# Optimization experiments

Measured on AMD Instinct MI355X. Metric: run time of the kernel, lower is better.

The kernel has to match this reference:

```python
import math
import jax, jax.numpy as jnp
import numpy as np

B, N, D = 8, 1024, 1024


def setup_inputs() -> dict:
    key = jax.random.key(0)
    ks = jax.random.split(key, 5)
    scale = 1.0 / math.sqrt(D)  # ~torch Linear init scale
    x = jax.random.normal(ks[0], (B, N, D), jnp.float32)
    Wq = jax.random.uniform(ks[1], (D, D), jnp.float32, -scale, scale)
    Wk = jax.random.uniform(ks[2], (D, D), jnp.float32, -scale, scale)
    Wv = jax.random.uniform(ks[3], (D, D), jnp.float32, -scale, scale)
    Ws = jax.random.uniform(ks[4], (D, 1), jnp.float32, -scale, scale)
    return {"x": x, "Wq": Wq, "Wk": Wk, "Wv": Wv, "Ws": Ws}


def reference(x, Wq, Wk, Wv, Ws):
    # projections
    Q = x @ Wq                      # [B, N, D]
    K = x @ Wk
    V = x @ Wv
    sigma = x @ Ws                  # [B, N, 1]
    sigma = jax.nn.sigmoid(sigma * 5.0) + 1e-5
    sigma = jnp.power(3.0, sigma) - 1.0

    # prior association: Gaussian kernel over |i-j| distances
    idx = jnp.arange(N, dtype=jnp.float32)
    dist = jnp.abs(idx[:, None] - idx[None, :])            # [N, N]
    inv_norm = 1.0 / (jnp.sqrt(2.0 * jnp.pi) * sigma)      # [B, N, 1]
    gaussian = inv_norm * jnp.exp(-0.5 * jnp.square(dist / sigma))  # [B, N, N]
    P = gaussian / gaussian.sum(axis=(1, 2), keepdims=True)

    # series association: softmax over the BATCH dim (dim=0), as in source
    scores = jnp.einsum('bnd,bmd->bnm', Q, K) / math.sqrt(D)  # [B, N, N]
    S = jax.nn.softmax(scores, axis=0)

    # reconstruction
    Z = jnp.einsum('bnm,bmd->bnd', S, V)                     # [B, N, D]
    return Z, P
```

## Files before the change

kernel.cpp:

```cpp
#include <hip/hip_runtime.h>


typedef __attribute__((ext_vector_type(8))) short bf16x8;
typedef __attribute__((ext_vector_type(4))) float f32x4;
typedef unsigned short ushort_t;

#define DI __device__ __forceinline__

constexpr long NN = 1024L * 1024L;
constexpr long ND = 1024L * 1024L;

DI ushort_t f2bf(float f) {
    unsigned int u = __float_as_uint(f);
    u = u + 0x7fffu + ((u >> 16) & 1u);
    return (ushort_t)(u >> 16);
}

template <int OUT_BF16>
DI void g3b_body(const ushort_t* __restrict__ Ab, const ushort_t* __restrict__ Bb,
                 void* __restrict__ Cb, int ldA, int ldB, int ldC,
                 float scale, int bx, int by, ushort_t* lds)
{
    constexpr int BUF   = 24576;
    constexpr int B_OFF = 8192;

    const int tid  = threadIdx.x;
    const int wave = tid >> 6;
    const int lane = tid & 63;
    const int wm   = wave >> 2;
    const int wn   = wave & 3;
    const int gm   = bx * 128;
    const int gn   = by * 256;

    const int srow = tid >> 3;
    const int scol = 8 * ((tid & 7) ^ (srow & 7));
    const int sdst = wave * 512;

    auto stageA = [&](int t, int d, int h) {
        const ushort_t* src = Ab + (long)(gm + h * 64 + srow) * ldA + t * 64 + scol;
        __builtin_amdgcn_global_load_lds(
            (const __attribute__((address_space(1))) void*)src,
            (__attribute__((address_space(3))) void*)(&lds[d * BUF + h * 4096 + sdst]),
            16, 0, 0);
    };
    auto stageB = [&](int t, int d, int h, int j) {
        const ushort_t* src = Bb + (long)(gn + h * 128 + j * 64 + srow) * ldB + t * 64 + scol;
        __builtin_amdgcn_global_load_lds(
            (const __attribute__((address_space(1))) void*)src,
            (__attribute__((address_space(3))) void*)(&lds[d * BUF + B_OFF + h * 8192 + j * 4096 + sdst]),
            16, 0, 0);
    };

    const int arow = wm * 64 + (lane & 15);
    const int brow = wn * 64 + (lane & 15);
    const int cs0 = (((lane >> 4) * 16) ^ ((lane & 7) << 4)) >> 1;
    const int cs1 = ((64 + (lane >> 4) * 16) ^ ((lane & 7) << 4)) >> 1;

    f32x4 acc[4][4];
#pragma unroll
    for (int m = 0; m < 4; ++m)
#pragma unroll
        for (int n = 0; n < 4; ++n) acc[m][n] = (f32x4){0.f, 0.f, 0.f, 0.f};

    stageA(0, 0, 0); stageA(0, 0, 1);
    stageB(0, 0, 0, 0); stageB(0, 0, 0, 1); stageB(0, 0, 1, 0); stageB(0, 0, 1, 1);
    stageA(1, 1, 0); stageA(1, 1, 1);
    stageB(1, 1, 0, 0); stageB(1, 1, 0, 1); stageB(1, 1, 1, 0); stageB(1, 1, 1, 1);
    asm volatile("s_waitcnt vmcnt(6)" ::: "memory");
    __builtin_amdgcn_s_barrier();
    __builtin_amdgcn_sched_barrier(0);

    int cur = 0;
    for (int t = 0; t < 16; ++t) {
        const int nxt = (cur == 0) ? 2 : cur - 1;
        const ushort_t* la = &lds[cur * BUF];
        const ushort_t* lb = &lds[cur * BUF + B_OFF];

        bf16x8 a[2][4], b[2][4];
#pragma unroll
        for (int mi = 0; mi < 4; ++mi) {
            a[0][mi] = *(const bf16x8*)&la[(arow + mi * 16) * 64 + cs0];
            a[1][mi] = *(const bf16x8*)&la[(arow + mi * 16) * 64 + cs1];
        }
#pragma unroll
        for (int ni = 0; ni < 2; ++ni) {
            b[0][ni] = *(const bf16x8*)&lb[(brow + ni * 16) * 64 + cs0];
            b[1][ni] = *(const bf16x8*)&lb[(brow + ni * 16) * 64 + cs1];
        }
        if (t < 14) {
            stageB(t + 2, nxt, 0, 0); stageB(t + 2, nxt, 0, 1);
            stageB(t + 2, nxt, 1, 0); stageB(t + 2, nxt, 1, 1);
        }
        __builtin_amdgcn_s_barrier();
        asm volatile("s_waitcnt lgkmcnt(0)" ::: "memory");
        __builtin_amdgcn_sched_barrier(0);
        __builtin_amdgcn_s_setprio(1);
#pragma unroll
        for (int mi = 0; mi < 4; ++mi)
#pragma unroll
            for (int ni = 0; ni < 2; ++ni) {
                acc[mi][ni] = __builtin_amdgcn_mfma_f32_16x16x32_bf16(a[0][mi], b[0][ni], acc[mi][ni], 0, 0, 0);
                acc[mi][ni] = __builtin_amdgcn_mfma_f32_16x16x32_bf16(a[1][mi], b[1][ni], acc[mi][ni], 0, 0, 0);
            }
        __builtin_amdgcn_s_setprio(0);
        __builtin_amdgcn_s_barrier();
        __builtin_amdgcn_sched_barrier(0);

#pragma unroll
        for (int ni = 2; ni < 4; ++ni) {
            b[0][ni] = *(const bf16x8*)&lb[(brow + ni * 16) * 64 + cs0];
            b[1][ni] = *(const bf16x8*)&lb[(brow + ni * 16) * 64 + cs1];
        }
        if (t < 14) { stageA(t + 2, nxt, 0); stageA(t + 2, nxt, 1); }
        __builtin_amdgcn_s_barrier();
        asm volatile("s_waitcnt lgkmcnt(0)" ::: "memory");
        if (t < 14) asm volatile("s_waitcnt vmcnt(6)" ::: "memory");
        else        asm volatile("s_waitcnt vmcnt(0)" ::: "memory");
        __builtin_amdgcn_sched_barrier(0);
        __builtin_amdgcn_s_setprio(1);
#pragma unroll
        for (int mi = 0; mi < 4; ++mi)
#pragma unroll
            for (int ni = 2; ni < 4; ++ni) {
                acc[mi][ni] = __builtin_amdgcn_mfma_f32_16x16x32_bf16(a[0][mi], b[0][ni], acc[mi][ni], 0, 0, 0);
                acc[mi][ni] = __builtin_amdgcn_mfma_f32_16x16x32_bf16(a[1][mi], b[1][ni], acc[mi][ni], 0, 0, 0);
            }
        __builtin_amdgcn_s_setprio(0);
        __builtin_amdgcn_s_barrier();
        __builtin_amdgcn_sched_barrier(0);

        cur = (cur == 2) ? 0 : cur + 1;
    }

    if (OUT_BF16) {
        ushort_t* el = lds;
#pragma unroll
        for (int mi = 0; mi < 4; ++mi)
#pragma unroll
            for (int ni = 0; ni < 4; ++ni)
#pragma unroll
                for (int r = 0; r < 4; ++r)
                    el[(wm * 64 + mi * 16 + (lane >> 4) * 4 + r) * 256 +
                       wn * 64 + ni * 16 + (lane & 15)] = f2bf(acc[mi][ni][r] * scale);
        __builtin_amdgcn_s_barrier();
        ushort_t* C = (ushort_t*)Cb;
#pragma unroll
        for (int rr = 0; rr < 8; ++rr) {
            const int row = rr * 16 + (tid >> 5);
            const int col = (tid & 31) * 8;
            *(bf16x8*)&C[(long)(gm + row) * ldC + gn + col] =
                *(const bf16x8*)&el[row * 256 + col];
        }
    } else {
        float* el = (float*)lds;
        float* C  = (float*)Cb;
#pragma unroll
        for (int h = 0; h < 2; ++h) {
            if (wm == h) {
#pragma unroll
                for (int mi = 0; mi < 4; ++mi)
#pragma unroll
                    for (int ni = 0; ni < 4; ++ni)
#pragma unroll
                        for (int r = 0; r < 4; ++r)
                            el[(mi * 16 + (lane >> 4) * 4 + r) * 256 +
                               wn * 64 + ni * 16 + (lane & 15)] = acc[mi][ni][r] * scale;
            }
            __builtin_amdgcn_s_barrier();
#pragma unroll
            for (int i = 0; i < 8; ++i) {
                const int cc  = i * 512 + tid;
                const int row = cc >> 6;
                const int c4  = (cc & 63) * 4;
                *(float4*)&C[(long)(gm + h * 64 + row) * ldC + gn + c4] =
                    *(const float4*)&el[row * 256 + c4];
            }
            __builtin_amdgcn_s_barrier();
        }
    }
}

template <int OUT_BF16>
__global__ __launch_bounds__(512, 2)
void gemm3b(const ushort_t* __restrict__ A, const ushort_t* __restrict__ B,
            void* __restrict__ Cout, int ldA, int ldB, int ldC,
            long sA, long sB, long sC, float scale,
            int n0, int n1, int xfirst)
{
    __shared__ ushort_t lds[3 * 24576];
    const int total = gridDim.x;
    const int lin   = blockIdx.x;
    const int swz   = (lin & 7) * (total >> 3) + (lin >> 3);
    const int c0    = swz % n0;
    const int rem   = swz / n0;
    const int c1    = rem % n1;
    const int bz    = rem / n1;
    const int bx    = xfirst ? c0 : c1;
    const int by    = xfirst ? c1 : c0;
    void* Cb = OUT_BF16 ? (void*)((ushort_t*)Cout + (long)bz * sC)
                        : (void*)((float*)Cout + (long)bz * sC);
    g3b_body<OUT_BF16>(A + (long)bz * sA, B + (long)bz * sB, Cb,
                       ldA, ldB, ldC, scale, bx, by, lds);
}

template <int OUT_BF16>
DI void g256_body(const ushort_t* __restrict__ Ab, const ushort_t* __restrict__ Bb,
                  void* __restrict__ Cb, int ldA, int ldB, int ldC,
                  float scale, int bx, int by, ushort_t* ldsp)
{
    constexpr int BUF   = 32768;
    constexpr int B_OFF = 16384;

    const int tid  = threadIdx.x;
    const int wave = tid >> 6;
    const int lane = tid & 63;
    const int wm   = wave >> 2;
    const int wn   = wave & 3;
    const int gm   = bx * 256;
    const int gn   = by * 256;

    const int srow = tid >> 3;
    const int scol = 8 * ((tid & 7) ^ (srow & 7));
    const int sdst = wave * 512;

    auto stage = [&](int t, int d, int op, int h) {
        const ushort_t* g  = op ? Bb : Ab;
        const int       ld = op ? ldB : ldA;
        const int       g0 = (op ? gn : gm) + h * 128;
#pragma unroll
        for (int j = 0; j < 2; ++j) {
            const ushort_t* src = g + (long)(g0 + j * 64 + srow) * ld + t * 64 + scol;
            __builtin_amdgcn_global_load_lds(
                (const __attribute__((address_space(1))) void*)src,
                (__attribute__((address_space(3))) void*)
                    (&ldsp[d * BUF + op * B_OFF + h * 8192 + j * 4096 + sdst]),
                16, 0, 0);
        }
    };

    const int arow = wm * 128 + (lane & 15);
    const int brow = wn * 64 + (lane & 15);
    const int cs0 = (((lane >> 4) * 16) ^ ((lane & 7) << 4)) >> 1;
    const int cs1 = ((64 + (lane >> 4) * 16) ^ ((lane & 7) << 4)) >> 1;

    f32x4 acc[8][4];
#pragma unroll
    for (int m = 0; m < 8; ++m)
#pragma unroll
        for (int n = 0; n < 4; ++n) acc[m][n] = (f32x4){0.f, 0.f, 0.f, 0.f};

    stage(0, 0, 0, 0); stage(0, 0, 0, 1); stage(0, 0, 1, 0); stage(0, 0, 1, 1);
    stage(1, 1, 0, 0); stage(1, 1, 0, 1); stage(1, 1, 1, 0); stage(1, 1, 1, 1);
    asm volatile("s_waitcnt vmcnt(8)" ::: "memory");
    __builtin_amdgcn_s_barrier();
    __builtin_amdgcn_sched_barrier(0);

    bf16x8 a[2][4], b0[2][2], b1[2][2];
#pragma unroll 2
    for (int t = 0; t < 16; ++t) {
        const int cur = t & 1;
        const ushort_t* la = &ldsp[cur * BUF];
        const ushort_t* lb = &ldsp[cur * BUF + B_OFF];

#pragma unroll
        for (int mi = 0; mi < 4; ++mi) {
            a[0][mi] = *(const bf16x8*)&la[(arow + mi * 16) * 64 + cs0];
            a[1][mi] = *(const bf16x8*)&la[(arow + mi * 16) * 64 + cs1];
        }
#pragma unroll
        for (int ni = 0; ni < 2; ++ni) {
            b0[0][ni] = *(const bf16x8*)&lb[(brow + ni * 16) * 64 + cs0];
            b0[1][ni] = *(const bf16x8*)&lb[(brow + ni * 16) * 64 + cs1];
        }
        __builtin_amdgcn_s_barrier();
        asm volatile("s_waitcnt lgkmcnt(0)" ::: "memory");
        __builtin_amdgcn_sched_barrier(0);
        __builtin_amdgcn_s_setprio(1);
#pragma unroll
        for (int mi = 0; mi < 4; ++mi)
#pragma unroll
            for (int ni = 0; ni < 2; ++ni) {
                acc[mi][ni] = __builtin_amdgcn_mfma_f32_16x16x32_bf16(a[0][mi], b0[0][ni], acc[mi][ni], 0, 0, 0);
                acc[mi][ni] = __builtin_amdgcn_mfma_f32_16x16x32_bf16(a[1][mi], b0[1][ni], acc[mi][ni], 0, 0, 0);
            }
        __builtin_amdgcn_s_setprio(0);
        __builtin_amdgcn_s_barrier();
        __builtin_amdgcn_sched_barrier(0);

#pragma unroll
        for (int ni = 0; ni < 2; ++ni) {
            b1[0][ni] = *(const bf16x8*)&lb[(brow + (ni + 2) * 16) * 64 + cs0];
            b1[1][ni] = *(const bf16x8*)&lb[(brow + (ni + 2) * 16) * 64 + cs1];
        }
        __builtin_amdgcn_s_barrier();
        asm volatile("s_waitcnt lgkmcnt(0)" ::: "memory");
        __builtin_amdgcn_sched_barrier(0);
        __builtin_amdgcn_s_setprio(1);
#pragma unroll
        for (int mi = 0; mi < 4; ++mi)
#pragma unroll
            for (int ni = 0; ni < 2; ++ni) {
                acc[mi][ni + 2] = __builtin_amdgcn_mfma_f32_16x16x32_bf16(a[0][mi], b1[0][ni], acc[mi][ni + 2], 0, 0, 0);
                acc[mi][ni + 2] = __builtin_amdgcn_mfma_f32_16x16x32_bf16(a[1][mi], b1[1][ni], acc[mi][ni + 2], 0, 0, 0);
            }
        __builtin_amdgcn_s_setprio(0);
        __builtin_amdgcn_s_barrier();
        __builtin_amdgcn_sched_barrier(0);

#pragma unroll
        for (int mi = 0; mi < 4; ++mi) {
            a[0][mi] = *(const bf16x8*)&la[(arow + (mi + 4) * 16) * 64 + cs0];
            a[1][mi] = *(const bf16x8*)&la[(arow + (mi + 4) * 16) * 64 + cs1];
        }
        if (t < 14) { stage(t + 2, cur, 1, 0); stage(t + 2, cur, 1, 1); }
        __builtin_amdgcn_s_barrier();
        asm volatile("s_waitcnt lgkmcnt(0)" ::: "memory");
        __builtin_amdgcn_sched_barrier(0);
        __builtin_amdgcn_s_setprio(1);
#pragma unroll
        for (int mi = 0; mi < 4; ++mi)
#pragma unroll
            for (int ni = 0; ni < 2; ++ni) {
                acc[mi + 4][ni + 2] = __builtin_amdgcn_mfma_f32_16x16x32_bf16(a[0][mi], b1[0][ni], acc[mi + 4][ni + 2], 0, 0, 0);
                acc[mi + 4][ni + 2] = __builtin_amdgcn_mfma_f32_16x16x32_bf16(a[1][mi], b1[1][ni], acc[mi + 4][ni + 2], 0, 0, 0);
            }
        __builtin_amdgcn_s_setprio(0);
        __builtin_amdgcn_s_barrier();
        __builtin_amdgcn_sched_barrier(0);

        if (t < 14) { stage(t + 2, cur, 0, 0); stage(t + 2, cur, 0, 1); }
        if (t < 14)       asm volatile("s_waitcnt vmcnt(8)" ::: "memory");
        else if (t == 14) asm volatile("s_waitcnt vmcnt(0)" ::: "memory");
        __builtin_amdgcn_sched_barrier(0);
        __builtin_amdgcn_s_setprio(1);
#pragma unroll
        for (int mi = 0; mi < 4; ++mi)
#pragma unroll
            for (int ni = 0; ni < 2; ++ni) {
                acc[mi + 4][ni] = __builtin_amdgcn_mfma_f32_16x16x32_bf16(a[0][mi], b0[0][ni], acc[mi + 4][ni], 0, 0, 0);
                acc[mi + 4][ni] = __builtin_amdgcn_mfma_f32_16x16x32_bf16(a[1][mi], b0[1][ni], acc[mi + 4][ni], 0, 0, 0);
            }
        __builtin_amdgcn_s_setprio(0);
        __builtin_amdgcn_s_barrier();
        __builtin_amdgcn_sched_barrier(0);
    }

    if (OUT_BF16) {
        ushort_t* el = ldsp;
#pragma unroll
        for (int mi = 0; mi < 8; ++mi)
#pragma unroll
            for (int ni = 0; ni < 4; ++ni)
#pragma unroll
                for (int r = 0; r < 4; ++r)
                    el[(wm * 128 + mi * 16 + (lane >> 4) * 4 + r) * 256 +
                       wn * 64 + ni * 16 + (lane & 15)] = f2bf(acc[mi][ni][r] * scale);
        __builtin_amdgcn_s_barrier();
        ushort_t* C = (ushort_t*)Cb;
#pragma unroll
        for (int i = 0; i < 16; ++i) {
            const int cc  = i * 512 + tid;
            const int row = cc >> 5;
            const int col = (cc & 31) * 8;
            *(bf16x8*)&C[(long)(gm + row) * ldC + gn + col] =
                *(const bf16x8*)&el[row * 256 + col];
        }
    } else {
        float* el = (float*)ldsp;
        float* C  = (float*)Cb;
#pragma unroll
        for (int h = 0; h < 2; ++h) {
            if (wm == h) {
#pragma unroll
                for (int mi = 0; mi < 8; ++mi)
#pragma unroll
                    for (int ni = 0; ni < 4; ++ni)
#pragma unroll
                        for (int r = 0; r < 4; ++r)
                            el[(mi * 16 + (lane >> 4) * 4 + r) * 256 +
                               wn * 64 + ni * 16 + (lane & 15)] = acc[mi][ni][r] * scale;
            }
            __builtin_amdgcn_s_barrier();
#pragma unroll
            for (int i = 0; i < 16; ++i) {
                const int cc  = i * 512 + tid;
                const int row = cc >> 6;
                const int c4  = (cc & 63) * 4;
                *(float4*)&C[(long)(gm + h * 128 + row) * ldC + gn + c4] =
                    *(const float4*)&el[row * 256 + c4];
            }
            __builtin_amdgcn_s_barrier();
        }
    }
}

__global__ __launch_bounds__(512)
void prep_g(const float* __restrict__ x, const float* __restrict__ Ws,
            const float* __restrict__ Wq, const float* __restrict__ Wk,
            const float* __restrict__ Wv,
            ushort_t* __restrict__ xh, float* __restrict__ sigma,
            float* __restrict__ rowsum,
            ushort_t* __restrict__ WvT, ushort_t* __restrict__ G)
{
    __shared__ char smem[20608];
    const int blk = blockIdx.x;
    const int tid = threadIdx.x;

    if (blk < 160) {
        const int wave = tid >> 6, lane = tid & 63;
        for (int row = blk * 8 + wave; row < 8192; row += 1280) {
            const float* xr = x + (long)row * 1024;
            float dot = 0.f;
#pragma unroll
            for (int c = 0; c < 4; ++c) {
                const int i = c * 256 + lane * 4;
                float4 v = *(const float4*)(xr + i);
                float4 w = *(const float4*)(Ws + i);
                dot += v.x * w.x + v.y * w.y + v.z * w.z + v.w * w.w;
                ushort4 o;
                o.x = f2bf(v.x); o.y = f2bf(v.y); o.z = f2bf(v.z); o.w = f2bf(v.w);
                *(ushort4*)(xh + (long)row * 1024 + i) = o;
            }
#pragma unroll
            for (int o = 32; o; o >>= 1) dot += __shfl_down(dot, o);
            float sg;
            if (lane == 0) {
                float s = 1.f / (1.f + __expf(-5.f * dot)) + 1e-5f;
                sg = exp2f(s * 1.5849625007211562f) - 1.f;
            }
            sg = __shfl(sg, 0);
            const int i = row & 1023;
            const float c = -0.5f / (sg * sg);
            float a = 0.f;
            for (int j = lane; j < 1024; j += 64) {
                float d = (float)(i - j);
                a += __expf(c * d * d);
            }
#pragma unroll
            for (int o = 32; o; o >>= 1) a += __shfl_down(a, o);
            if (lane == 0) {
                sigma[row]  = sg;
                rowsum[row] = (0.3989422804014327f / sg) * a;
            }
        }
    } else if (blk < 192) {
        float (*s)[65] = (float(*)[65])smem;
        const int r = tid >> 4, c4 = (tid & 15) * 4;
#pragma unroll
        for (int it = 0; it < 8; ++it) {
            const int tile = (blk - 160) * 8 + it;
            const int tr = (tile >> 4) * 64, tc = (tile & 15) * 64;
#pragma unroll
            for (int rr = r; rr < 64; rr += 32) {
                float4 v = *(const float4*)(Wv + (long)(tr + rr) * 1024 + tc + c4);
                s[rr][c4] = v.x; s[rr][c4 + 1] = v.y; s[rr][c4 + 2] = v.z; s[rr][c4 + 3] = v.w;
            }
            __syncthreads();
#pragma unroll
            for (int rr = r; rr < 64; rr += 32) {
                ushort4 o;
                o.x = f2bf(s[c4][rr]);     o.y = f2bf(s[c4 + 1][rr]);
                o.z = f2bf(s[c4 + 2][rr]); o.w = f2bf(s[c4 + 3][rr]);
                *(ushort4*)(WvT + (long)(tc + rr) * 1024 + tr + c4) = o;
            }
            __syncthreads();
        }
    } else {
        ushort_t* sA = (ushort_t*)smem;
        ushort_t* sB = sA + 5120;
        const int g  = blk - 192;
        const int gm = (g >> 3) * 128, gn = (g & 7) * 128;
        const int wave = tid >> 6, lane = tid & 63;
        const int wm = wave >> 2, wn = wave & 3;
        const int lrow = tid >> 3, lcol = (tid & 7) * 4;
        const float* A0 = Wk + (long)(gm + lrow) * 1024 + lcol;
        const float* A1 = Wk + (long)(gm + 64 + lrow) * 1024 + lcol;
        const float* B0 = Wq + (long)(gn + lrow) * 1024 + lcol;
        const float* B1 = Wq + (long)(gn + 64 + lrow) * 1024 + lcol;

        f32x4 acc[4][2];
#pragma unroll
        for (int m = 0; m < 4; ++m)
#pragma unroll
            for (int n = 0; n < 2; ++n) acc[m][n] = (f32x4){0.f, 0.f, 0.f, 0.f};

        auto wr = [&](float4 a0, float4 a1, float4 b0, float4 b1) {
            ushort4 o;
            o.x = f2bf(a0.x); o.y = f2bf(a0.y); o.z = f2bf(a0.z); o.w = f2bf(a0.w);
            *(ushort4*)&sA[lrow * 40 + lcol] = o;
            o.x = f2bf(a1.x); o.y = f2bf(a1.y); o.z = f2bf(a1.z); o.w = f2bf(a1.w);
            *(ushort4*)&sA[(64 + lrow) * 40 + lcol] = o;
            o.x = f2bf(b0.x); o.y = f2bf(b0.y); o.z = f2bf(b0.z); o.w = f2bf(b0.w);
            *(ushort4*)&sB[lrow * 40 + lcol] = o;
            o.x = f2bf(b1.x); o.y = f2bf(b1.y); o.z = f2bf(b1.z); o.w = f2bf(b1.w);
            *(ushort4*)&sB[(64 + lrow) * 40 + lcol] = o;
        };
        auto mm = [&]() {
            bf16x8 af[4], bfv[2];
#pragma unroll
            for (int mi = 0; mi < 4; ++mi)
                af[mi] = *(const bf16x8*)&sA[(wm * 64 + mi * 16 + (lane & 15)) * 40 + (lane >> 4) * 8];
#pragma unroll
            for (int ni = 0; ni < 2; ++ni)
                bfv[ni] = *(const bf16x8*)&sB[(wn * 32 + ni * 16 + (lane & 15)) * 40 + (lane >> 4) * 8];
#pragma unroll
            for (int mi = 0; mi < 4; ++mi)
#pragma unroll
                for (int ni = 0; ni < 2; ++ni)
                    acc[mi][ni] = __builtin_amdgcn_mfma_f32_16x16x32_bf16(af[mi], bfv[ni], acc[mi][ni], 0, 0, 0);
        };

        float4 a0A = *(const float4*)(A0);      float4 a1A = *(const float4*)(A1);
        float4 b0A = *(const float4*)(B0);      float4 b1A = *(const float4*)(B1);
        float4 a0B = *(const float4*)(A0 + 32); float4 a1B = *(const float4*)(A1 + 32);
        float4 b0B = *(const float4*)(B0 + 32); float4 b1B = *(const float4*)(B1 + 32);

        for (int k0 = 0; k0 < 1024; k0 += 64) {
            wr(a0A, a1A, b0A, b1A);
            if (k0 < 960) {
                a0A = *(const float4*)(A0 + k0 + 64); a1A = *(const float4*)(A1 + k0 + 64);
                b0A = *(const float4*)(B0 + k0 + 64); b1A = *(const float4*)(B1 + k0 + 64);
            }
            __syncthreads();
            mm();
            __syncthreads();
            wr(a0B, a1B, b0B, b1B);
            if (k0 < 928) {
                a0B = *(const float4*)(A0 + k0 + 96); a1B = *(const float4*)(A1 + k0 + 96);
                b0B = *(const float4*)(B0 + k0 + 96); b1B = *(const float4*)(B1 + k0 + 96);
            }
            __syncthreads();
            mm();
            __syncthreads();
        }
#pragma unroll
        for (int mi = 0; mi < 4; ++mi)
#pragma unroll
            for (int ni = 0; ni < 2; ++ni)
#pragma unroll
                for (int r = 0; r < 4; ++r)
                    G[(long)(gm + wm * 64 + mi * 16 + (lane >> 4) * 4 + r) * 1024 +
                      gn + wn * 32 + ni * 16 + (lane & 15)] = f2bf(acc[mi][ni][r]);
    }
}

__global__ __launch_bounds__(512, 2)
void sc_vt(const ushort_t* __restrict__ xqh, const ushort_t* __restrict__ xh,
           float* __restrict__ scores,
           const ushort_t* __restrict__ WvT, ushort_t* __restrict__ VTall)
{
    __shared__ ushort_t lds[2 * 32768];
    const int lin = blockIdx.x;
    if (lin < 128) {
        const int bz = lin & 7;
        const int t  = lin >> 3;
        g256_body<0>(xqh + (long)bz * ND, xh + (long)bz * ND,
                     (void*)(scores + (long)bz * NN),
                     1024, 1024, 1024, 0.03125f, t & 3, t >> 2, lds);
    } else {
        const int l  = lin - 128;
        const int l2 = (l & 7) * 16 + (l >> 3);
        g256_body<1>(WvT, xh, (void*)VTall,
                     1024, 1024, 8192, 1.f, l2 & 3, l2 >> 2, lds);
    }
}

__global__ __launch_bounds__(512, 2)
void sv_prior(const ushort_t* __restrict__ S, const ushort_t* __restrict__ VTall,
              float* __restrict__ Z, const float* __restrict__ sigma,
              const float* __restrict__ rowsum, float* __restrict__ P)
{
    __shared__ ushort_t lds[2 * 32768];
    const int lin = blockIdx.x;
    const int tid = threadIdx.x;
    if (lin < 128) {
        const int bz = lin & 7;
        const int t  = lin >> 3;
        g256_body<0>(S + (long)bz * NN, VTall + bz * 1024,
                     (void*)(Z + (long)bz * ND),
                     1024, 8192, 1024, 1.f, t & 3, t >> 2, lds);
    } else {
        const int l = lin - 128;
        const int b = l >> 4;
        float* sred = (float*)lds;
        float a = rowsum[b * 1024 + tid] + rowsum[b * 1024 + 512 + tid];
        sred[tid] = a; __syncthreads();
        for (int o = 256; o; o >>= 1) { if (tid < o) sred[tid] += sred[tid + o]; __syncthreads(); }
        const float bs = sred[0];
        const int r0 = (l & 15) * 64;
#pragma unroll
        for (int it = 0; it < 32; ++it) {
            const int e   = it * 512 + tid;
            const int row = r0 + (e >> 8);
            const int j4  = (e & 255) * 4;
            const float sg  = sigma[(b << 10) + row];
            const float c   = -0.5f / (sg * sg);
            const float inv = 0.3989422804014327f / (sg * bs);
            float4 o;
            float d;
            d = (float)(row - j4);       o.x = inv * __expf(c * d * d);
            d = (float)(row - j4 - 1);   o.y = inv * __expf(c * d * d);
            d = (float)(row - j4 - 2);   o.z = inv * __expf(c * d * d);
            d = (float)(row - j4 - 3);   o.w = inv * __expf(c * d * d);
            *(float4*)&P[(long)b * NN + (long)row * 1024 + j4] = o;
        }
    }
}

__global__ void softmax_batch(const float* __restrict__ scores, ushort_t* __restrict__ S)
{
    const long idx = (long)blockIdx.x * 256 + threadIdx.x;
    float v[8], m = -1e30f;
#pragma unroll
    for (int b = 0; b < 8; ++b) { v[b] = scores[(long)b * NN + idx]; m = fmaxf(m, v[b]); }
    float sum = 0.f;
#pragma unroll
    for (int b = 0; b < 8; ++b) { v[b] = __expf(v[b] - m); sum += v[b]; }
    const float inv = 1.f / sum;
#pragma unroll
    for (int b = 0; b < 8; ++b) S[(long)b * NN + idx] = f2bf(v[b] * inv);
}

extern "C" void kernel_launch(void* const* d_in, const int* in_sizes, int n_in,
                              void* d_out, int out_size, void* d_ws, size_t ws_size,
                              hipStream_t stream)
{
    const float* x  = (const float*)d_in[0];
    const float* Wq = (const float*)d_in[1];
    const float* Wk = (const float*)d_in[2];
    const float* Wv = (const float*)d_in[3];
    const float* Ws = (const float*)d_in[4];
    float* Zout = (float*)d_out;
    float* Pout = Zout + 8 * ND;

    char* base = (char*)d_ws;
    size_t off = 0;
    auto alloc = [&](size_t bytes) {
        void* p = base + off;
        off = (off + bytes + 255) & ~(size_t)255;
        return p;
    };
    ushort_t* xh    = (ushort_t*)alloc(8192L * 1024 * 2);
    ushort_t* G     = (ushort_t*)alloc(NN * 2);
    ushort_t* WvT   = (ushort_t*)alloc(NN * 2);
    ushort_t* xqh   = (ushort_t*)alloc(8192L * 1024 * 2);
    ushort_t* VTall = (ushort_t*)alloc(1024L * 8192 * 2);
    float* sigma    = (float*)alloc(8192 * 4);
    float* rowsum   = (float*)alloc(8192 * 4);
    float*    scores = Pout;
    ushort_t* Sh     = xh;

    prep_g<<<256, 512, 0, stream>>>(x, Ws, Wq, Wk, Wv, xh, sigma, rowsum, WvT, G);
    gemm3b<1><<<256, 512, 0, stream>>>(
        xh, G, xqh, 1024, 1024, 1024, 0, 0, 0, 1.f, 4, 64, 0);
    sc_vt<<<256, 512, 0, stream>>>(xqh, xh, scores, WvT, VTall);
    softmax_batch<<<4096, 256, 0, stream>>>(scores, Sh);
    sv_prior<<<256, 512, 0, stream>>>(Sh, VTall, Zout, sigma, rowsum, Pout);
}
```

Baseline: 133.0 us.

## Restructure GEMM main loop to cut barriers and overlap LDS reads with MFMA

Reworks the per-k-step schedule of the bf16 MFMA GEMM mainloop. All B fragments and both halves of A are held in separate registers so fragment loads can be issued together. Most of the per-quadrant s_barrier/lgkmcnt(0) waits are dropped, leaving barriers only around the global-to-LDS staging points. The aim is less synchronisation stall and more overlap of LDS reads with MFMA work, at the cost of extra VGPRs for the separate a0/a1 fragments and a tighter reliance on compiler-inserted waits for correctness.

```diff
diff --git a/kernel.cpp b/kernel.cpp
--- a/kernel.cpp
+++ b/kernel.cpp
@@ -255,92 +255,82 @@
     __builtin_amdgcn_s_barrier();
     __builtin_amdgcn_sched_barrier(0);
 
-    bf16x8 a[2][4], b0[2][2], b1[2][2];
 #pragma unroll 2
     for (int t = 0; t < 16; ++t) {
         const int cur = t & 1;
         const ushort_t* la = &ldsp[cur * BUF];
         const ushort_t* lb = &ldsp[cur * BUF + B_OFF];
 
+        bf16x8 a0[2][4], a1[2][4], b0[2][2], b1[2][2];
 #pragma unroll
         for (int mi = 0; mi < 4; ++mi) {
-            a[0][mi] = *(const bf16x8*)&la[(arow + mi * 16) * 64 + cs0];
-            a[1][mi] = *(const bf16x8*)&la[(arow + mi * 16) * 64 + cs1];
+            a0[0][mi] = *(const bf16x8*)&la[(arow + mi * 16) * 64 + cs0];
+            a0[1][mi] = *(const bf16x8*)&la[(arow + mi * 16) * 64 + cs1];
         }
 #pragma unroll
         for (int ni = 0; ni < 2; ++ni) {
             b0[0][ni] = *(const bf16x8*)&lb[(brow + ni * 16) * 64 + cs0];
             b0[1][ni] = *(const bf16x8*)&lb[(brow + ni * 16) * 64 + cs1];
-        }
-        __builtin_amdgcn_s_barrier();
-        asm volatile("s_waitcnt lgkmcnt(0)" ::: "memory");
-        __builtin_amdgcn_sched_barrier(0);
-        __builtin_amdgcn_s_setprio(1);
-#pragma unroll
-        for (int mi = 0; mi < 4; ++mi)
-#pragma unroll
-            for (int ni = 0; ni < 2; ++ni) {
-                acc[mi][ni] = __builtin_amdgcn_mfma_f32_16x16x32_bf16(a[0][mi], b0[0][ni], acc[mi][ni], 0, 0, 0);
-                acc[mi][ni] = __builtin_amdgcn_mfma_f32_16x16x32_bf16(a[1][mi], b0[1][ni], acc[mi][ni], 0, 0, 0);
-            }
-        __builtin_amdgcn_s_setprio(0);
-        __builtin_amdgcn_s_barrier();
-        __builtin_amdgcn_sched_barrier(0);
-
-#pragma unroll
-        for (int ni = 0; ni < 2; ++ni) {
             b1[0][ni] = *(const bf16x8*)&lb[(brow + (ni + 2) * 16) * 64 + cs0];
             b1[1][ni] = *(const bf16x8*)&lb[(brow + (ni + 2) * 16) * 64 + cs1];
         }
-        __builtin_amdgcn_s_barrier();
-        asm volatile("s_waitcnt lgkmcnt(0)" ::: "memory");
-        __builtin_amdgcn_sched_barrier(0);
         __builtin_amdgcn_s_setprio(1);
 #pragma unroll
         for (int mi = 0; mi < 4; ++mi)
 #pragma unroll
             for (int ni = 0; ni < 2; ++ni) {
-                acc[mi][ni + 2] = __builtin_amdgcn_mfma_f32_16x16x32_bf16(a[0][mi], b1[0][ni], acc[mi][ni + 2], 0, 0, 0);
-                acc[mi][ni + 2] = __builtin_amdgcn_mfma_f32_16x16x32_bf16(a[1][mi], b1[1][ni], acc[mi][ni + 2], 0, 0, 0);
+                acc[mi][ni] = __builtin_amdgcn_mfma_f32_16x16x32_bf16(a0[0][mi], b0[0][ni], acc[mi][ni], 0, 0, 0);
+                acc[mi][ni] = __builtin_amdgcn_mfma_f32_16x16x32_bf16(a0[1][mi], b0[1][ni], acc[mi][ni], 0, 0, 0);
             }
         __builtin_amdgcn_s_setprio(0);
-        __builtin_amdgcn_s_barrier();
-        __builtin_amdgcn_sched_barrier(0);
 
 #pragma unroll
         for (int mi = 0; mi < 4; ++mi) {
-            a[0][mi] = *(const bf16x8*)&la[(arow + (mi + 4) * 16) * 64 + cs0];
-            a[1][mi] = *(const bf16x8*)&la[(arow + (mi + 4) * 16) * 64 + cs1];
-        }
+            a1[0][mi] = *(const bf16x8*)&la[(arow + (mi + 4) * 16) * 64 + cs0];
+            a1[1][mi] = *(const bf16x8*)&la[(arow + (mi + 4) * 16) * 64 + cs1];
+        }
+        __builtin_amdgcn_s_setprio(1);
+#pragma unroll
+        for (int mi = 0; mi < 4; ++mi)
+#pragma unroll
+            for (int ni = 0; ni < 2; ++ni) {
+                acc[mi][ni + 2] = __builtin_amdgcn_mfma_f32_16x16x32_bf16(a0[0][mi], b1[0][ni], acc[mi][ni + 2], 0, 0, 0);
+                acc[mi][ni + 2] = __builtin_amdgcn_mfma_f32_16x16x32_bf16(a0[1][mi], b1[1][ni], acc[mi][ni + 2], 0, 0, 0);
+            }
+        __builtin_amdgcn_s_setprio(0);
+
+        __builtin_amdgcn_sched_barrier(0);
+        __builtin_amdgcn_s_barrier();
+        __builtin_amdgcn_sched_barrier(0);
         if (t < 14) { stage(t + 2, cur, 1, 0); stage(t + 2, cur, 1, 1); }
-        __builtin_amdgcn_s_barrier();
-        asm volatile("s_waitcnt lgkmcnt(0)" ::: "memory");
-        __builtin_amdgcn_sched_barrier(0);
+
         __builtin_amdgcn_s_setprio(1);
 #pragma unroll
         for (int mi = 0; mi < 4; ++mi)
 #pragma unroll
             for (int ni = 0; ni < 2; ++ni) {
-                acc[mi + 4][ni + 2] = __builtin_amdgcn_mfma_f32_16x16x32_bf16(a[0][mi], b1[0][ni], acc[mi + 4][ni + 2], 0, 0, 0);
-                acc[mi + 4][ni + 2] = __builtin_amdgcn_mfma_f32_16x16x32_bf16(a[1][mi], b1[1][ni], acc[mi + 4][ni + 2], 0, 0, 0);
+                acc[mi + 4][ni + 2] = __builtin_amdgcn_mfma_f32_16x16x32_bf16(a1[0][mi], b1[0][ni], acc[mi + 4][ni + 2], 0, 0, 0);
+                acc[mi + 4][ni + 2] = __builtin_amdgcn_mfma_f32_16x16x32_bf16(a1[1][mi], b1[1][ni], acc[mi + 4][ni + 2], 0, 0, 0);
             }
         __builtin_amdgcn_s_setprio(0);
-        __builtin_amdgcn_s_barrier();
-        __builtin_amdgcn_sched_barrier(0);
-
+
+        __builtin_amdgcn_sched_barrier(0);
+        __builtin_amdgcn_s_barrier();
+        __builtin_amdgcn_sched_barrier(0);
         if (t < 14) { stage(t + 2, cur, 0, 0); stage(t + 2, cur, 0, 1); }
+
+        __builtin_amdgcn_s_setprio(1);
+#pragma unroll
+        for (int mi = 0; mi < 4; ++mi)
+#pragma unroll
+            for (int ni = 0; ni < 2; ++ni) {
+                acc[mi + 4][ni] = __builtin_amdgcn_mfma_f32_16x16x32_bf16(a1[0][mi], b0[0][ni], acc[mi + 4][ni], 0, 0, 0);
+                acc[mi + 4][ni] = __builtin_amdgcn_mfma_f32_16x16x32_bf16(a1[1][mi], b0[1][ni], acc[mi + 4][ni], 0, 0, 0);
+            }
+        __builtin_amdgcn_s_setprio(0);
         if (t < 14)       asm volatile("s_waitcnt vmcnt(8)" ::: "memory");
         else if (t == 14) asm volatile("s_waitcnt vmcnt(0)" ::: "memory");
         __builtin_amdgcn_sched_barrier(0);
-        __builtin_amdgcn_s_setprio(1);
-#pragma unroll
-        for (int mi = 0; mi < 4; ++mi)
-#pragma unroll
-            for (int ni = 0; ni < 2; ++ni) {
-                acc[mi + 4][ni] = __builtin_amdgcn_mfma_f32_16x16x32_bf16(a[0][mi], b0[0][ni], acc[mi + 4][ni], 0, 0, 0);
-                acc[mi + 4][ni] = __builtin_amdgcn_mfma_f32_16x16x32_bf16(a[1][mi], b0[1][ni], acc[mi + 4][ni], 0, 0, 0);
-            }
-        __builtin_amdgcn_s_setprio(0);
         __builtin_amdgcn_s_barrier();
         __builtin_amdgcn_sched_barrier(0);
     }
```

Result: slower. 158.4 us (+19.1%).

## Move prior computation into softmax kernel and run S@V as standalone gemm

Applied to the files above, without the earlier changes.

The Gaussian prior P is now computed in the same launch as the batch softmax, using 1024 extra small blocks. The S@V GEMM becomes its own gemm3b launch instead of sharing a kernel with the prior. Because P is written while scores are still being read, scores now get their own workspace buffer instead of aliasing the P output. The aim is to hide the bandwidth-bound prior writes behind the softmax and give the GEMM a uniform launch. The cost is an extra 32 MB workspace buffer and a different GEMM tile configuration.

```diff
diff --git a/kernel.cpp b/kernel.cpp
--- a/kernel.cpp
+++ b/kernel.cpp
@@ -565,32 +565,37 @@
     }
 }
 
-__global__ __launch_bounds__(512, 2)
-void sv_prior(const ushort_t* __restrict__ S, const ushort_t* __restrict__ VTall,
-              float* __restrict__ Z, const float* __restrict__ sigma,
-              const float* __restrict__ rowsum, float* __restrict__ P)
+__global__ __launch_bounds__(256)
+void softmax_prior(const float* __restrict__ scores, ushort_t* __restrict__ S,
+                   const float* __restrict__ sigma, const float* __restrict__ rowsum,
+                   float* __restrict__ P)
 {
-    __shared__ ushort_t lds[2 * 32768];
-    const int lin = blockIdx.x;
+    __shared__ float sred[256];
+    const int blk = blockIdx.x;
     const int tid = threadIdx.x;
-    if (lin < 128) {
-        const int bz = lin & 7;
-        const int t  = lin >> 3;
-        g256_body<0>(S + (long)bz * NN, VTall + bz * 1024,
-                     (void*)(Z + (long)bz * ND),
-                     1024, 8192, 1024, 1.f, t & 3, t >> 2, lds);
+    if (blk < 4096) {
+        const long idx = (long)blk * 256 + tid;
+        float v[8], m = -1e30f;
+#pragma unroll
+        for (int b = 0; b < 8; ++b) { v[b] = scores[(long)b * NN + idx]; m = fmaxf(m, v[b]); }
+        float sum = 0.f;
+#pragma unroll
+        for (int b = 0; b < 8; ++b) { v[b] = __expf(v[b] - m); sum += v[b]; }
+        const float inv = 1.f / sum;
+#pragma unroll
+        for (int b = 0; b < 8; ++b) S[(long)b * NN + idx] = f2bf(v[b] * inv);
     } else {
-        const int l = lin - 128;
-        const int b = l >> 4;
-        float* sred = (float*)lds;
-        float a = rowsum[b * 1024 + tid] + rowsum[b * 1024 + 512 + tid];
+        const int l = blk - 4096;
+        const int b = l >> 7;
+        float a = rowsum[b * 1024 + tid]       + rowsum[b * 1024 + 256 + tid] +
+                  rowsum[b * 1024 + 512 + tid] + rowsum[b * 1024 + 768 + tid];
         sred[tid] = a; __syncthreads();
-        for (int o = 256; o; o >>= 1) { if (tid < o) sred[tid] += sred[tid + o]; __syncthreads(); }
+        for (int o = 128; o; o >>= 1) { if (tid < o) sred[tid] += sred[tid + o]; __syncthreads(); }
         const float bs = sred[0];
-        const int r0 = (l & 15) * 64;
-#pragma unroll
-        for (int it = 0; it < 32; ++it) {
-            const int e   = it * 512 + tid;
+        const int r0 = (l & 127) * 8;
+#pragma unroll
+        for (int it = 0; it < 8; ++it) {
+            const int e   = it * 256 + tid;
             const int row = r0 + (e >> 8);
             const int j4  = (e & 255) * 4;
             const float sg  = sigma[(b << 10) + row];
@@ -607,20 +612,6 @@
     }
 }
 
-__global__ void softmax_batch(const float* __restrict__ scores, ushort_t* __restrict__ S)
-{
-    const long idx = (long)blockIdx.x * 256 + threadIdx.x;
-    float v[8], m = -1e30f;
-#pragma unroll
-    for (int b = 0; b < 8; ++b) { v[b] = scores[(long)b * NN + idx]; m = fmaxf(m, v[b]); }
-    float sum = 0.f;
-#pragma unroll
-    for (int b = 0; b < 8; ++b) { v[b] = __expf(v[b] - m); sum += v[b]; }
-    const float inv = 1.f / sum;
-#pragma unroll
-    for (int b = 0; b < 8; ++b) S[(long)b * NN + idx] = f2bf(v[b] * inv);
-}
-
 extern "C" void kernel_launch(void* const* d_in, const int* in_sizes, int n_in,
                               void* d_out, int out_size, void* d_ws, size_t ws_size,
                               hipStream_t stream)
@@ -640,20 +631,21 @@
         off = (off + bytes + 255) & ~(size_t)255;
         return p;
     };
-    ushort_t* xh    = (ushort_t*)alloc(8192L * 1024 * 2);
-    ushort_t* G     = (ushort_t*)alloc(NN * 2);
-    ushort_t* WvT   = (ushort_t*)alloc(NN * 2);
-    ushort_t* xqh   = (ushort_t*)alloc(8192L * 1024 * 2);
-    ushort_t* VTall = (ushort_t*)alloc(1024L * 8192 * 2);
-    float* sigma    = (float*)alloc(8192 * 4);
-    float* rowsum   = (float*)alloc(8192 * 4);
-    float*    scores = Pout;
+    ushort_t* xh     = (ushort_t*)alloc(8192L * 1024 * 2);
+    ushort_t* G      = (ushort_t*)alloc(NN * 2);
+    ushort_t* WvT    = (ushort_t*)alloc(NN * 2);
+    ushort_t* xqh    = (ushort_t*)alloc(8192L * 1024 * 2);
+    ushort_t* VTall  = (ushort_t*)alloc(1024L * 8192 * 2);
+    float*    scores = (float*)alloc(8L * NN * 4);
+    float* sigma     = (float*)alloc(8192 * 4);
+    float* rowsum    = (float*)alloc(8192 * 4);
     ushort_t* Sh     = xh;
 
     prep_g<<<256, 512, 0, stream>>>(x, Ws, Wq, Wk, Wv, xh, sigma, rowsum, WvT, G);
     gemm3b<1><<<256, 512, 0, stream>>>(
         xh, G, xqh, 1024, 1024, 1024, 0, 0, 0, 1.f, 4, 64, 0);
     sc_vt<<<256, 512, 0, stream>>>(xqh, xh, scores, WvT, VTall);
-    softmax_batch<<<4096, 256, 0, stream>>>(scores, Sh);
-    sv_prior<<<256, 512, 0, stream>>>(Sh, VTall, Zout, sigma, rowsum, Pout);
-}
+    softmax_prior<<<5120, 256, 0, stream>>>(scores, Sh, sigma, rowsum, Pout);
+    gemm3b<0><<<256, 512, 0, stream>>>(
+        Sh, VTall, Zout, 1024, 8192, 1024, NN, 1024, ND, 1.f, 8, 4, 1);
+}
```

New measurement: 124.8 us. -6.1%, faster.
